# Performance work log

Measured on AMD Instinct MI355X. Metric: run time of the kernel, lower is better.

The kernel has to match this reference:

```python
import jax, jax.numpy as jnp
import numpy as np

N = 1536      # n_nodes (A.shape[0])
P_DIM = 32    # p: number of eigenvectors kept
FTS = 32      # MLP hidden width
L = 3         # number of adjacency powers / MLPs


def setup_inputs() -> dict:
    rng = np.random.default_rng(0)
    # Random sparse symmetric adjacency, as in graph denoising setups.
    A = rng.normal(size=(N, N)).astype(np.float32)
    A = (A + A.T) * 0.5
    mask = rng.random((N, N)) < 0.05
    mask = mask | mask.T
    A = A * mask
    # __init__: eigh, normalize by |lambdas[0]|, keep first p eigenvectors.
    lambdas, V = np.linalg.eigh(A)
    A_norm = (A / np.abs(lambdas[0])).astype(np.float32)
    P = V[:, :P_DIM].astype(np.float32)

    key = jax.random.key(0)
    k1, k2 = jax.random.split(key)
    # Per-power tiny MLPs: Linear(p,fts) -> ReLU -> Linear(fts,1), stacked over L.
    W1 = jax.random.normal(k1, (L, P_DIM, FTS), jnp.float32) / np.sqrt(P_DIM)
    b1 = jnp.zeros((L, FTS), jnp.float32)
    W2 = jax.random.normal(k2, (L, FTS, 1), jnp.float32) / np.sqrt(FTS)
    b2 = jnp.zeros((L, 1), jnp.float32)
    return {"A_norm": jnp.asarray(A_norm), "P": jnp.asarray(P),
            "W1": W1, "b1": b1, "W2": W2, "b2": b2}


def reference(A_norm, P, W1, b1, W2, b2):
    # create_conv_matrix: Conv[i,j] = sum_l A^l[i,j] * MLP_l(P[i] - P[j]).
    # Multiplying by A^l zeroes the non-edges of the l-th power, which is
    # exactly the masked per-edge gather/MLP/scatter loop of the original.
    n = A_norm.shape[0]
    diff = P[:, None, :] - P[None, :, :]              # [N, N, p] pairwise gather
    A_l = jnp.eye(n, dtype=A_norm.dtype)              # A^0
    conv = jnp.zeros((n, n), A_norm.dtype)
    for l in range(W1.shape[0]):                      # L is small & static
        h = jax.nn.relu(diff @ W1[l] + b1[l])         # [N, N, fts]
        m = (h @ W2[l])[..., 0] + b2[l][0]            # [N, N] per-edge scalar
        conv = conv + A_l * m                         # fused scatter-add
        A_l = A_l @ A_norm                            # next power
    return conv
```

## Files before the change

### kernel.cpp

```cpp
#include <hip/hip_runtime.h>
#include <hip/hip_fp16.h>

#define NN 1536
#define FDIM 32
#define TG 96
#define KS 64
#define NTH 12
#define NPMAX 768

typedef __attribute__((ext_vector_type(4))) int i32x4;
typedef __attribute__((ext_vector_type(4))) float f32x4;
typedef _Float16 h16x2 __attribute__((ext_vector_type(2)));

typedef __attribute__((address_space(3))) unsigned char as3_u8;
typedef __attribute__((address_space(1))) unsigned char as1_u8;

__device__ __forceinline__ void gload_lds16(const void* g, void* l) {
    __builtin_amdgcn_global_load_lds((const as1_u8*)g, (as3_u8*)l, 16, 0, 0);
}

__device__ __forceinline__ float reduce_pmax(const float* __restrict__ pmax) {
    const int lane = threadIdx.x & 63;
    float m = 0.f;
#pragma unroll
    for (int t = 0; t < NPMAX / 64; ++t) m = fmaxf(m, pmax[lane + t * 64]);
#pragma unroll
    for (int k = 32; k >= 1; k >>= 1) m = fmaxf(m, __shfl_xor(m, k, 64));
    return m;
}

__global__ __launch_bounds__(256) void gud_absmax(const float* __restrict__ A,
                                                  float* __restrict__ pmax) {
    __shared__ float red[4];
    const float4* A4 = reinterpret_cast<const float4*>(A);
    const int base = blockIdx.x * 768 + threadIdx.x;
    float m = 0.f;
#pragma unroll
    for (int t = 0; t < 3; ++t) {
        float4 v = A4[base + t * 256];
        m = fmaxf(m, fmaxf(fmaxf(fabsf(v.x), fabsf(v.y)),
                           fmaxf(fabsf(v.z), fabsf(v.w))));
    }
#pragma unroll
    for (int k = 32; k >= 1; k >>= 1)
        m = fmaxf(m, __shfl_xor(m, k, 64));
    if ((threadIdx.x & 63) == 0) red[threadIdx.x >> 6] = m;
    __syncthreads();
    if (threadIdx.x == 0)
        pmax[blockIdx.x] = fmaxf(fmaxf(red[0], red[1]), fmaxf(red[2], red[3]));
}

__global__ __launch_bounds__(256) void gud_quantprep(
        const float* __restrict__ A,
        const float* __restrict__ pmax,
        unsigned char* __restrict__ qH,
        unsigned char* __restrict__ qL,
        const float* __restrict__ P,
        const float* __restrict__ W1,
        const float* __restrict__ b1,
        _Float16* __restrict__ QIh,
        _Float16* __restrict__ RJh) {
    const int b = blockIdx.x;
    if (b < NN * NN / 1024) {
        const float inv = 32639.0f / reduce_pmax(pmax);
        int gid = b * 256 + threadIdx.x;
        float4 v = reinterpret_cast<const float4*>(A)[gid];
        unsigned hw = 0, lw = 0;
        float elems[4] = {v.x, v.y, v.z, v.w};
#pragma unroll
        for (int e = 0; e < 4; ++e) {
            int q  = (int)rintf(fminf(fmaxf(elems[e] * inv, -32639.f), 32639.f));
            int hh = (q + 128) >> 8;
            int ll = q - (hh << 8);
            hw |= ((unsigned)(hh & 0xff)) << (8 * e);
            lw |= ((unsigned)(ll & 0xff)) << (8 * e);
        }
        reinterpret_cast<unsigned*>(qH)[gid] = hw;
        reinterpret_cast<unsigned*>(qL)[gid] = lw;
    } else {
        int gid = (b - NN * NN / 1024) * 256 + threadIdx.x;
        int i  = gid >> 6;
        int lf = gid & 63;
        int l  = (lf >> 5) + 1;
        int f  = lf & 31;
        const float* prow = P + i * FDIM;
        const float* wp   = W1 + l * FDIM * FDIM + f;
        float q = 0.f;
#pragma unroll
        for (int c = 0; c < FDIM; ++c) q = fmaf(prow[c], wp[c * FDIM], q);
        QIh[i * 64 + lf] = (_Float16)(q + b1[l * FDIM + f]);
        RJh[i * 64 + lf] = (_Float16)(-q);
    }
}

__global__ __launch_bounds__(512, 1) void gud_fused(
        const unsigned char* __restrict__ qH,
        const unsigned char* __restrict__ qL,
        const float* __restrict__ pmax,
        const float* __restrict__ A,
        const _Float16* __restrict__ QIh,
        const _Float16* __restrict__ RJh,
        const float* __restrict__ b1,
        const float* __restrict__ W2,
        const float* __restrict__ b2,
        float* __restrict__ out) {
    __shared__ alignas(16) char sb0[49152];
    __shared__ alignas(16) char sb1[49152];
    __shared__ alignas(16) char sb2[49152];

    const int tid  = threadIdx.x;
    const int lane = tid & 63;
    const int w    = tid >> 6;
    const int kh   = w >> 2;
    const int sub  = w & 3;
    const int wr   = sub >> 1, wc = sub & 1;

    const int lin = blockIdx.x;
    const int swz = (lin & 7) * 32 + (lin >> 3);
    const int by  = swz >> 4, bx = swz & 15;
    const int i0  = by * TG, j0 = bx * TG;

    const unsigned char* src = (sub & 1) ? qL : qH;
    const int rowbase = (sub < 2) ? i0 : j0;
    const int khbyte  = kh * (NN / 2);
    int goffs[6];
#pragma unroll
    for (int s = 0; s < 6; ++s) {
        int rt    = 16 * s + (lane >> 2);
        int chunk = (lane & 3) ^ ((rt >> 1) & 3);
        goffs[s]  = (rowbase + rt) * NN + khbyte + chunk * 16;
    }

    const int hbase = kh * 24576;
    int aoff[3], boff[3];
    const int kb = lane >> 4;
#pragma unroll
    for (int m = 0; m < 3; ++m) {
        int ra  = wr * 48 + m * 16 + (lane & 15);
        aoff[m] = hbase + ra * 64 + ((kb ^ ((ra >> 1) & 3)) * 16);
        int rb  = wc * 48 + m * 16 + (lane & 15);
        boff[m] = hbase + 12288 + rb * 64 + ((kb ^ ((rb >> 1) & 3)) * 16);
    }

    i32x4 accH[3][3], accX[3][3];
#pragma unroll
    for (int m = 0; m < 3; ++m)
#pragma unroll
        for (int n = 0; n < 3; ++n) {
            accH[m][n] = (i32x4){0, 0, 0, 0};
            accX[m][n] = (i32x4){0, 0, 0, 0};
        }

    auto compute = [&](const char (&buf)[49152]) {
        i32x4 hA[3], lA[3], hB[3], lB[3];
#pragma unroll
        for (int m = 0; m < 3; ++m) {
            hA[m] = *(const i32x4*)(&buf[aoff[m]]);
            lA[m] = *(const i32x4*)(&buf[aoff[m] + 6144]);
            hB[m] = *(const i32x4*)(&buf[boff[m]]);
            lB[m] = *(const i32x4*)(&buf[boff[m] + 6144]);
        }
        __builtin_amdgcn_s_setprio(1);
#pragma unroll
        for (int m = 0; m < 3; ++m)
#pragma unroll
            for (int n = 0; n < 3; ++n) {
                accH[m][n] = __builtin_amdgcn_mfma_i32_16x16x64_i8(hA[m], hB[n], accH[m][n], 0, 0, 0);
                accX[m][n] = __builtin_amdgcn_mfma_i32_16x16x64_i8(hA[m], lB[n], accX[m][n], 0, 0, 0);
                accX[m][n] = __builtin_amdgcn_mfma_i32_16x16x64_i8(lA[m], hB[n], accX[m][n], 0, 0, 0);
            }
        __builtin_amdgcn_s_setprio(0);
    };

#pragma unroll
    for (int s = 0; s < 6; ++s)
        gload_lds16((const char*)src + goffs[s], sb0 + w * 6144 + s * 1024);
#pragma unroll
    for (int s = 0; s < 6; ++s)
        gload_lds16((const char*)src + goffs[s] + KS, sb1 + w * 6144 + s * 1024);

#define GSTEP(BC, BS, KT, VC) do {                                           \
    asm volatile("s_waitcnt vmcnt(" #VC ")" ::: "memory");                   \
    __builtin_amdgcn_s_barrier();                                            \
    if ((KT) < NTH) {                                                        \
        _Pragma("unroll")                                                    \
        for (int s = 0; s < 6; ++s)                                          \
            gload_lds16((const char*)src + goffs[s] + (KT) * KS,             \
                        BS + w * 6144 + s * 1024);                           \
    }                                                                        \
    compute(BC);                                                             \
} while (0)

    GSTEP(sb0, sb2, 2, 6);
    GSTEP(sb1, sb0, 3, 6);
    GSTEP(sb2, sb1, 4, 6);
    GSTEP(sb0, sb2, 5, 6);
    GSTEP(sb1, sb0, 6, 6);
    GSTEP(sb2, sb1, 7, 6);
    GSTEP(sb0, sb2, 8, 6);
    GSTEP(sb1, sb0, 9, 6);
    GSTEP(sb2, sb1, 10, 6);
    GSTEP(sb0, sb2, 11, 6);
    GSTEP(sb1, sb0, 12, 6);
    GSTEP(sb2, sb1, 13, 0);
#undef GSTEP

    const float sq = reduce_pmax(pmax) / 32639.0f;
    const float c1 = sq * sq * 65536.0f;
    const float c2 = sq * sq * 256.0f;
    f32x4 af[3][3];
#pragma unroll
    for (int m = 0; m < 3; ++m)
#pragma unroll
        for (int n = 0; n < 3; ++n)
#pragma unroll
            for (int r = 0; r < 4; ++r)
                af[m][n][r] = c1 * (float)accH[m][n][r] + c2 * (float)accX[m][n][r];

    if (kh == 1) {
        char* pbase = sb1 + sub * 9216 + lane * 144;
#pragma unroll
        for (int m = 0; m < 3; ++m)
#pragma unroll
            for (int n = 0; n < 3; ++n)
                *(f32x4*)(pbase + (m * 3 + n) * 16) = af[m][n];
    }
    if (w < 4) {
#pragma unroll
        for (int sl = 0; sl < 3; ++sl) {
            int base = (w * 3 + sl) * 64;
            int idx  = base + lane;
            int c    = idx / 96;
            int row  = idx - c * 96;
            gload_lds16(QIh + (size_t)(i0 + row) * 64 + c * 8, sb0 + base * 16);
        }
    } else {
#pragma unroll
        for (int sl = 0; sl < 3; ++sl) {
            int base = ((w - 4) * 3 + sl) * 64;
            int idx  = base + lane;
            int c    = idx / 96;
            int row  = idx - c * 96;
            gload_lds16(RJh + (size_t)(j0 + row) * 64 + c * 8, sb0 + 12288 + base * 16);
        }
    }

    const int crow = (lane >> 4) * 4;
    const int ccol = lane & 15;
    int il[3], jl[3];
#pragma unroll
    for (int m = 0; m < 3; ++m) il[m] = wr * 48 + m * 16 + crow;
#pragma unroll
    for (int n = 0; n < 3; ++n) jl[n] = wc * 48 + n * 16 + ccol;

    float av[3][3][4];
    if (kh == 0) {
#pragma unroll
        for (int m = 0; m < 3; ++m)
#pragma unroll
            for (int n = 0; n < 3; ++n)
#pragma unroll
                for (int r = 0; r < 4; ++r)
                    av[m][n][r] = A[(size_t)(i0 + il[m] + r) * NN + j0 + jl[n]];
    }

    __syncthreads();

    if (kh == 1) return;

    {
        const char* pbase = sb1 + sub * 9216 + lane * 144;
#pragma unroll
        for (int m = 0; m < 3; ++m)
#pragma unroll
            for (int n = 0; n < 3; ++n)
                af[m][n] += *(const f32x4*)(pbase + (m * 3 + n) * 16);
    }

    const char* QIl = sb0;
    const char* RJl = sb0 + 12288;

    float c0 = b2[0];
#pragma unroll
    for (int f = 0; f < FDIM; ++f) c0 = fmaf(fmaxf(b1[f], 0.f), W2[f], c0);
    const float bb1 = b2[1], bb2 = b2[2];

    h16x2 w2h[32];
#pragma unroll
    for (int k = 0; k < 32; ++k) {
        h16x2 t; t.x = (_Float16)W2[32 + 2 * k]; t.y = (_Float16)W2[33 + 2 * k];
        w2h[k] = t;
    }

    float mm[3][3][4];
#pragma unroll
    for (int m = 0; m < 3; ++m)
#pragma unroll
        for (int n = 0; n < 3; ++n)
#pragma unroll
            for (int r = 0; r < 4; ++r) mm[m][n][r] = 0.f;
#pragma unroll
    for (int c = 0; c < 4; ++c) {
        uint4 rv[3];
#pragma unroll
        for (int n = 0; n < 3; ++n)
            rv[n] = *(const uint4*)(RJl + (c * 96 + jl[n]) * 16);
        uint4 qv[3][4];
#pragma unroll
        for (int m = 0; m < 3; ++m)
#pragma unroll
            for (int r = 0; r < 4; ++r)
                qv[m][r] = *(const uint4*)(QIl + (c * 96 + il[m] + r) * 16);
#pragma unroll
        for (int m = 0; m < 3; ++m)
#pragma unroll
            for (int n = 0; n < 3; ++n) {
                const unsigned* ru = (const unsigned*)&rv[n];
#pragma unroll
                for (int r = 0; r < 4; ++r) {
                    const unsigned* qu = (const unsigned*)&qv[m][r];
                    float acc_f = mm[m][n][r];
#pragma unroll
                    for (int e = 0; e < 4; ++e) {
                        h16x2 q = __builtin_bit_cast(h16x2, qu[e]);
                        h16x2 j = __builtin_bit_cast(h16x2, ru[e]);
                        h16x2 h = q + j;
                        h16x2 z = {(_Float16)0, (_Float16)0};
                        h = __builtin_elementwise_max(h, z);
                        acc_f = __builtin_amdgcn_fdot2(h, w2h[c * 4 + e], acc_f, false);
                    }
                    mm[m][n][r] = acc_f;
                }
            }
    }
#pragma unroll
    for (int m = 0; m < 3; ++m)
#pragma unroll
        for (int n = 0; n < 3; ++n)
#pragma unroll
            for (int r = 0; r < 4; ++r)
                av[m][n][r] *= (mm[m][n][r] + bb1);

#pragma unroll
    for (int m = 0; m < 3; ++m)
#pragma unroll
        for (int n = 0; n < 3; ++n)
#pragma unroll
            for (int r = 0; r < 4; ++r) mm[m][n][r] = 0.f;
#pragma unroll
    for (int c = 4; c < 8; ++c) {
        uint4 rv[3];
#pragma unroll
        for (int n = 0; n < 3; ++n)
            rv[n] = *(const uint4*)(RJl + (c * 96 + jl[n]) * 16);
        uint4 qv[3][4];
#pragma unroll
        for (int m = 0; m < 3; ++m)
#pragma unroll
            for (int r = 0; r < 4; ++r)
                qv[m][r] = *(const uint4*)(QIl + (c * 96 + il[m] + r) * 16);
#pragma unroll
        for (int m = 0; m < 3; ++m)
#pragma unroll
            for (int n = 0; n < 3; ++n) {
                const unsigned* ru = (const unsigned*)&rv[n];
#pragma unroll
                for (int r = 0; r < 4; ++r) {
                    const unsigned* qu = (const unsigned*)&qv[m][r];
                    float acc_f = mm[m][n][r];
#pragma unroll
                    for (int e = 0; e < 4; ++e) {
                        h16x2 q = __builtin_bit_cast(h16x2, qu[e]);
                        h16x2 j = __builtin_bit_cast(h16x2, ru[e]);
                        h16x2 h = q + j;
                        h16x2 z = {(_Float16)0, (_Float16)0};
                        h = __builtin_elementwise_max(h, z);
                        acc_f = __builtin_amdgcn_fdot2(h, w2h[c * 4 + e], acc_f, false);
                    }
                    mm[m][n][r] = acc_f;
                }
            }
    }

#pragma unroll
    for (int m = 0; m < 3; ++m)
#pragma unroll
        for (int n = 0; n < 3; ++n)
#pragma unroll
            for (int r = 0; r < 4; ++r) {
                float v = av[m][n][r] + af[m][n][r] * (mm[m][n][r] + bb2);
                int gi = i0 + il[m] + r;
                int gj = j0 + jl[n];
                if (gi == gj) v += c0;
                out[(size_t)gi * NN + gj] = v;
            }
}

extern "C" void kernel_launch(void* const* d_in, const int* in_sizes, int n_in,
                              void* d_out, int out_size, void* d_ws, size_t ws_size,
                              hipStream_t stream) {
    const float* A  = (const float*)d_in[0];
    const float* P  = (const float*)d_in[1];
    const float* W1 = (const float*)d_in[2];
    const float* b1 = (const float*)d_in[3];
    const float* W2 = (const float*)d_in[4];
    const float* b2 = (const float*)d_in[5];
    float* out = (float*)d_out;

    unsigned char* qH = (unsigned char*)d_ws;
    unsigned char* qL = qH + (size_t)NN * NN;
    _Float16* QIh = (_Float16*)(qL + (size_t)NN * NN);
    _Float16* RJh = QIh + (size_t)NN * 64;
    float* pmax = (float*)(RJh + (size_t)NN * 64);

    gud_absmax<<<dim3(NPMAX), 256, 0, stream>>>(A, pmax);
    gud_quantprep<<<dim3(NN * NN / 1024 + NN * 64 / 256), 256, 0, stream>>>(
        A, pmax, qH, qL, P, W1, b1, QIh, RJh);
    gud_fused<<<dim3((NN / TG) * (NN / TG)), 512, 0, stream>>>(
        qH, qL, pmax, A, QIh, RJh, b1, W2, b2, out);
}
```

Measured before the change: 42.16 us.

## Drop split-K warps; give each wave a private barrier-free triple-buffered pipeline

The fused kernel previously ran 8 waves split into two K-halves, with shared LDS tiles, block barriers every K step, and a cross-wave LDS reduction of partial sums. It now runs 4 waves, each loading its own 48-row A and B slices over the full K range into a private triple-buffered LDS region, with only vmcnt waits and no barriers. This removes per-step block synchronisation and the split-K reduction. The cost is duplicated global-to-LDS traffic, since waves sharing a row or column each load it, and half the waves per block to hide latency.

```diff
diff --git a/kernel.cpp b/kernel.cpp
--- a/kernel.cpp
+++ b/kernel.cpp
@@ -5,7 +5,7 @@
 #define FDIM 32
 #define TG 96
 #define KS 64
-#define NTH 12
+#define NTK 24
 #define NPMAX 768
 
 typedef __attribute__((ext_vector_type(4))) int i32x4;
@@ -93,7 +93,7 @@
     }
 }
 
-__global__ __launch_bounds__(512, 1) void gud_fused(
+__global__ __launch_bounds__(256, 1) void gud_fused(
         const unsigned char* __restrict__ qH,
         const unsigned char* __restrict__ qL,
         const float* __restrict__ pmax,
@@ -104,42 +104,41 @@
         const float* __restrict__ W2,
         const float* __restrict__ b2,
         float* __restrict__ out) {
-    __shared__ alignas(16) char sb0[49152];
-    __shared__ alignas(16) char sb1[49152];
-    __shared__ alignas(16) char sb2[49152];
+    __shared__ alignas(16) char smem[147456];
 
     const int tid  = threadIdx.x;
     const int lane = tid & 63;
     const int w    = tid >> 6;
-    const int kh   = w >> 2;
-    const int sub  = w & 3;
-    const int wr   = sub >> 1, wc = sub & 1;
+    const int wr   = w >> 1, wc = w & 1;
 
     const int lin = blockIdx.x;
     const int swz = (lin & 7) * 32 + (lin >> 3);
     const int by  = swz >> 4, bx = swz & 15;
     const int i0  = by * TG, j0 = bx * TG;
 
-    const unsigned char* src = (sub & 1) ? qL : qH;
-    const int rowbase = (sub < 2) ? i0 : j0;
-    const int khbyte  = kh * (NN / 2);
-    int goffs[6];
-#pragma unroll
-    for (int s = 0; s < 6; ++s) {
-        int rt    = 16 * s + (lane >> 2);
-        int chunk = (lane & 3) ^ ((rt >> 1) & 3);
-        goffs[s]  = (rowbase + rt) * NN + khbyte + chunk * 16;
-    }
-
-    const int hbase = kh * 24576;
+    char* priv = smem + w * 36864;
+
+    const unsigned char* csrc[4] = {qH, qL, qH, qL};
+    int goffs[4][3];
+#pragma unroll
+    for (int cls = 0; cls < 4; ++cls) {
+        const int rowbase = (cls < 2) ? (i0 + wr * 48) : (j0 + wc * 48);
+#pragma unroll
+        for (int s = 0; s < 3; ++s) {
+            int lr    = s * 16 + (lane >> 2);
+            int chunk = (lane & 3) ^ ((lr >> 1) & 3);
+            goffs[cls][s] = (rowbase + lr) * NN + chunk * 16;
+        }
+    }
+
     int aoff[3], boff[3];
     const int kb = lane >> 4;
 #pragma unroll
     for (int m = 0; m < 3; ++m) {
-        int ra  = wr * 48 + m * 16 + (lane & 15);
-        aoff[m] = hbase + ra * 64 + ((kb ^ ((ra >> 1) & 3)) * 16);
-        int rb  = wc * 48 + m * 16 + (lane & 15);
-        boff[m] = hbase + 12288 + rb * 64 + ((kb ^ ((rb >> 1) & 3)) * 16);
+        int lr  = m * 16 + (lane & 15);
+        int sw  = (kb ^ ((lr >> 1) & 3)) * 16;
+        aoff[m] = lr * 64 + sw;
+        boff[m] = lr * 64 + sw;
     }
 
     i32x4 accH[3][3], accX[3][3];
@@ -151,14 +150,24 @@
             accX[m][n] = (i32x4){0, 0, 0, 0};
         }
 
-    auto compute = [&](const char (&buf)[49152]) {
+    auto stage = [&](char* buf, int kt) {
+        const int kbyte = kt * KS;
+#pragma unroll
+        for (int cls = 0; cls < 4; ++cls)
+#pragma unroll
+            for (int s = 0; s < 3; ++s)
+                gload_lds16((const char*)csrc[cls] + goffs[cls][s] + kbyte,
+                            buf + cls * 3072 + s * 1024);
+    };
+
+    auto compute = [&](const char* buf) {
         i32x4 hA[3], lA[3], hB[3], lB[3];
 #pragma unroll
         for (int m = 0; m < 3; ++m) {
-            hA[m] = *(const i32x4*)(&buf[aoff[m]]);
-            lA[m] = *(const i32x4*)(&buf[aoff[m] + 6144]);
-            hB[m] = *(const i32x4*)(&buf[boff[m]]);
-            lB[m] = *(const i32x4*)(&buf[boff[m] + 6144]);
+            hA[m] = *(const i32x4*)(buf + 0    + aoff[m]);
+            lA[m] = *(const i32x4*)(buf + 3072 + aoff[m]);
+            hB[m] = *(const i32x4*)(buf + 6144 + boff[m]);
+            lB[m] = *(const i32x4*)(buf + 9216 + boff[m]);
         }
         __builtin_amdgcn_s_setprio(1);
 #pragma unroll
@@ -172,38 +181,18 @@
         __builtin_amdgcn_s_setprio(0);
     };
 
-#pragma unroll
-    for (int s = 0; s < 6; ++s)
-        gload_lds16((const char*)src + goffs[s], sb0 + w * 6144 + s * 1024);
-#pragma unroll
-    for (int s = 0; s < 6; ++s)
-        gload_lds16((const char*)src + goffs[s] + KS, sb1 + w * 6144 + s * 1024);
-
-#define GSTEP(BC, BS, KT, VC) do {                                           \
-    asm volatile("s_waitcnt vmcnt(" #VC ")" ::: "memory");                   \
-    __builtin_amdgcn_s_barrier();                                            \
-    if ((KT) < NTH) {                                                        \
-        _Pragma("unroll")                                                    \
-        for (int s = 0; s < 6; ++s)                                          \
-            gload_lds16((const char*)src + goffs[s] + (KT) * KS,             \
-                        BS + w * 6144 + s * 1024);                           \
-    }                                                                        \
-    compute(BC);                                                             \
-} while (0)
-
-    GSTEP(sb0, sb2, 2, 6);
-    GSTEP(sb1, sb0, 3, 6);
-    GSTEP(sb2, sb1, 4, 6);
-    GSTEP(sb0, sb2, 5, 6);
-    GSTEP(sb1, sb0, 6, 6);
-    GSTEP(sb2, sb1, 7, 6);
-    GSTEP(sb0, sb2, 8, 6);
-    GSTEP(sb1, sb0, 9, 6);
-    GSTEP(sb2, sb1, 10, 6);
-    GSTEP(sb0, sb2, 11, 6);
-    GSTEP(sb1, sb0, 12, 6);
-    GSTEP(sb2, sb1, 13, 0);
-#undef GSTEP
+    stage(priv, 0);
+    stage(priv + 12288, 1);
+
+    for (int kt = 0; kt < NTK; ++kt) {
+        if (kt < NTK - 1)
+            asm volatile("s_waitcnt vmcnt(12)" ::: "memory");
+        else
+            asm volatile("s_waitcnt vmcnt(0)" ::: "memory");
+        if (kt + 2 < NTK)
+            stage(priv + ((kt + 2) % 3) * 12288, kt + 2);
+        compute(priv + (kt % 3) * 12288);
+    }
 
     const float sq = reduce_pmax(pmax) / 32639.0f;
     const float c1 = sq * sq * 65536.0f;
@@ -217,32 +206,23 @@
             for (int r = 0; r < 4; ++r)
                 af[m][n][r] = c1 * (float)accH[m][n][r] + c2 * (float)accX[m][n][r];
 
-    if (kh == 1) {
-        char* pbase = sb1 + sub * 9216 + lane * 144;
-#pragma unroll
-        for (int m = 0; m < 3; ++m)
-#pragma unroll
-            for (int n = 0; n < 3; ++n)
-                *(f32x4*)(pbase + (m * 3 + n) * 16) = af[m][n];
-    }
-    if (w < 4) {
-#pragma unroll
-        for (int sl = 0; sl < 3; ++sl) {
-            int base = (w * 3 + sl) * 64;
-            int idx  = base + lane;
-            int c    = idx / 96;
-            int row  = idx - c * 96;
-            gload_lds16(QIh + (size_t)(i0 + row) * 64 + c * 8, sb0 + base * 16);
-        }
-    } else {
-#pragma unroll
-        for (int sl = 0; sl < 3; ++sl) {
-            int base = ((w - 4) * 3 + sl) * 64;
-            int idx  = base + lane;
-            int c    = idx / 96;
-            int row  = idx - c * 96;
-            gload_lds16(RJh + (size_t)(j0 + row) * 64 + c * 8, sb0 + 12288 + base * 16);
-        }
+    __syncthreads();
+
+#pragma unroll
+    for (int sl = 0; sl < 3; ++sl) {
+        int base = (w * 3 + sl) * 64;
+        int idx  = base + lane;
+        int c    = idx / 96;
+        int row  = idx - c * 96;
+        gload_lds16(QIh + (size_t)(i0 + row) * 64 + c * 8, smem + base * 16);
+    }
+#pragma unroll
+    for (int sl = 0; sl < 3; ++sl) {
+        int base = (w * 3 + sl) * 64;
+        int idx  = base + lane;
+        int c    = idx / 96;
+        int row  = idx - c * 96;
+        gload_lds16(RJh + (size_t)(j0 + row) * 64 + c * 8, smem + 12288 + base * 16);
     }
 
     const int crow = (lane >> 4) * 4;
@@ -254,31 +234,18 @@
     for (int n = 0; n < 3; ++n) jl[n] = wc * 48 + n * 16 + ccol;
 
     float av[3][3][4];
-    if (kh == 0) {
-#pragma unroll
-        for (int m = 0; m < 3; ++m)
-#pragma unroll
-            for (int n = 0; n < 3; ++n)
-#pragma unroll
-                for (int r = 0; r < 4; ++r)
-                    av[m][n][r] = A[(size_t)(i0 + il[m] + r) * NN + j0 + jl[n]];
-    }
+#pragma unroll
+    for (int m = 0; m < 3; ++m)
+#pragma unroll
+        for (int n = 0; n < 3; ++n)
+#pragma unroll
+            for (int r = 0; r < 4; ++r)
+                av[m][n][r] = A[(size_t)(i0 + il[m] + r) * NN + j0 + jl[n]];
 
     __syncthreads();
 
-    if (kh == 1) return;
-
-    {
-        const char* pbase = sb1 + sub * 9216 + lane * 144;
-#pragma unroll
-        for (int m = 0; m < 3; ++m)
-#pragma unroll
-            for (int n = 0; n < 3; ++n)
-                af[m][n] += *(const f32x4*)(pbase + (m * 3 + n) * 16);
-    }
-
-    const char* QIl = sb0;
-    const char* RJl = sb0 + 12288;
+    const char* QIl = smem;
+    const char* RJl = smem + 12288;
 
     float c0 = b2[0];
 #pragma unroll
@@ -416,6 +383,6 @@
     gud_absmax<<<dim3(NPMAX), 256, 0, stream>>>(A, pmax);
     gud_quantprep<<<dim3(NN * NN / 1024 + NN * 64 / 256), 256, 0, stream>>>(
         A, pmax, qH, qL, P, W1, b1, QIh, RJh);
-    gud_fused<<<dim3((NN / TG) * (NN / TG)), 512, 0, stream>>>(
+    gud_fused<<<dim3((NN / TG) * (NN / TG)), 256, 0, stream>>>(
         qH, qL, pmax, A, QIh, RJh, b1, W2, b2, out);
 }
```

New measurement: 45.57 us. +8.1%, slower.
